# Kernel tuning notes

Hardware: AMD Instinct MI355X
Metric: run time of the kernel (lower is better)

The kernel has to match this reference:

```python
import jax, jax.numpy as jnp
import numpy as np
import math

NUM_HEADS = 16
SEGMENT_SIZE = 256
DILATION_RATE = 2


def _hilbert_curve(n):
    if n == 1:
        return [(0, 0)]
    m = n // 2
    sub = _hilbert_curve(m)
    pts = [(y, x) for (x, y) in sub]
    pts += [(x, y + m) for (x, y) in sub]
    pts += [(x + m, y + m) for (x, y) in sub]
    pts += [(m - 1 - y + m, m - 1 - x) for (x, y) in sub]
    return pts


def generate_hilbert_curve_mapping(seq_len):
    grid = 2 ** int(math.ceil(math.log2(math.sqrt(seq_len))))
    pts = _hilbert_curve(grid)
    lin2hil = np.zeros(seq_len, dtype=np.int32)
    for h_idx, (x, y) in enumerate(pts[:seq_len]):
        lin = y * grid + x
        if lin < seq_len:
            lin2hil[lin] = h_idx
    return lin2hil


def setup_inputs() -> dict:
    key = jax.random.key(0)
    k1, k2, k3 = jax.random.split(key, 3)
    B, S, H = 1, 4096, 2048
    scale = H ** -0.5
    x = jax.random.normal(k1, (B, S, H), dtype=jnp.float32)
    w_qkv = jax.random.normal(k2, (3 * H, H), dtype=jnp.float32) * scale
    w_out = jax.random.normal(k3, (H, H), dtype=jnp.float32) * scale
    hilbert_map = jnp.asarray(generate_hilbert_curve_mapping(S))
    return {"x": x, "w_qkv": w_qkv, "w_out": w_out, "hilbert_map": hilbert_map}


def _kv_positions(S, seg, dil):
    # Union of per-segment dilated positions: seg_start + j*dil (< segment end).
    seg_starts = np.arange(0, S, seg)
    within = np.arange(0, seg, dil)
    return jnp.asarray((seg_starts[:, None] + within[None, :]).reshape(-1))


def reference(x, w_qkv, w_out, hilbert_map):
    B, S, H = x.shape
    nh = NUM_HEADS
    hd = H // nh
    qkv = x @ w_qkv.T                              # [B,S,3H]
    qkv = qkv.reshape(B, S, 3, nh, hd).transpose(2, 0, 3, 1, 4)  # [3,B,nh,S,hd]
    q, k, v = qkv[0], qkv[1], qkv[2]

    kv_pos = _kv_positions(S, SEGMENT_SIZE, DILATION_RATE)  # [Nk]
    gathered = hilbert_map[kv_pos]                 # Hilbert-mapped KV indices
    kg = k[:, :, gathered, :]                      # [B,nh,Nk,hd]
    vg = v[:, :, gathered, :]

    scale = 1.0 / jnp.sqrt(jnp.float32(hd))
    scores = jnp.einsum("bhmd,bhnd->bhmn", q, kg) * scale
    p = jax.nn.softmax(scores, axis=-1)
    acc = jnp.einsum("bhmn,bhnd->bhmd", p, vg)     # [B,nh,S,hd]

    # Scatter: out[:, :, hilbert_map[m], :] = acc[:, :, m, :]
    out = jnp.zeros_like(acc).at[:, :, hilbert_map, :].set(acc)
    out = out.transpose(0, 2, 1, 3).reshape(B, S, H)
    return out @ w_out.T
```

## Files before the change

kernel.cpp:

```cpp
#include <hip/hip_runtime.h>
#include <math.h>

#define S_LEN 4096
#define HID   2048
#define NH    16
#define HD    128
#define NKV   2048
#define KT    64
#define QBLK  256
#define NT    (NKV / KT)
#define QSCALE 0.12754103668587426f

typedef __attribute__((ext_vector_type(8))) _Float16 half8;
typedef __attribute__((ext_vector_type(4))) _Float16 half4;
typedef __attribute__((ext_vector_type(2))) __fp16 fp16x2;
typedef __attribute__((ext_vector_type(4))) float f32x4;
typedef __attribute__((ext_vector_type(16))) float f32x16;

#define GLB_AS __attribute__((address_space(1)))
#define LDS_AS __attribute__((address_space(3)))

__device__ __forceinline__ void gload16(const void* g, void* l) {
  __builtin_amdgcn_global_load_lds((GLB_AS const void*)g, (LDS_AS void*)l, 16, 0, 0);
}

__device__ __forceinline__ unsigned pkrtz(float a, float b) {
  union { fp16x2 h; unsigned u; } cv;
  cv.h = __builtin_amdgcn_cvt_pkrtz(a, b);
  return cv.u;
}

__global__ void k_build_idx(const int* __restrict__ hmap, int* __restrict__ gidx) {
  int i = blockIdx.x * 256 + threadIdx.x;
  if (i < NKV) gidx[i] = hmap[2 * i];
}

__global__ void k_cvt_f16(const float* __restrict__ src, _Float16* __restrict__ dst, int n8) {
  int i = blockIdx.x * 256 + threadIdx.x;
  if (i < n8) {
    float4 a = ((const float4*)src)[2 * i];
    float4 b = ((const float4*)src)[2 * i + 1];
    half8 h;
    h[0] = (_Float16)a.x; h[1] = (_Float16)a.y; h[2] = (_Float16)a.z; h[3] = (_Float16)a.w;
    h[4] = (_Float16)b.x; h[5] = (_Float16)b.y; h[6] = (_Float16)b.z; h[7] = (_Float16)b.w;
    ((half8*)dst)[i] = h;
  }
}

template<int MODE>
__global__ __launch_bounds__(256)
void k_gemm2(const _Float16* __restrict__ A, const _Float16* __restrict__ B,
             void* __restrict__ Cv, int M, int N, int K,
             const int* __restrict__ arow,
             char* __restrict__ kimg, char* __restrict__ vtimg)
{
  __shared__ __align__(16) char Asl[16384];
  __shared__ __align__(16) char Bsl[16384];
  const int tid = threadIdx.x;
  const int w = tid >> 6, lane = tid & 63;
  const int l15 = lane & 15, l4 = lane >> 4;
  const int m0 = blockIdx.y * 128, n0 = blockIdx.x * 128;
  const int wr = w >> 1, wc = w & 1;

  const int srow  = lane >> 3;
  const int kso   = ((lane & 7) ^ srow) * 8;
  const _Float16* Ap[4];
  const _Float16* Bp[4];
#pragma unroll
  for (int q = 0; q < 4; ++q) {
    int arel = m0 + 32 * w + 8 * q + srow;
    int ra = arow ? arow[arel] : arel;
    Ap[q] = A + (size_t)ra * K + kso;
    Bp[q] = B + (size_t)(n0 + 32 * w + 8 * q + srow) * K + kso;
  }

  f32x4 acc[4][4];
#pragma unroll
  for (int i = 0; i < 4; ++i)
#pragma unroll
    for (int j = 0; j < 4; ++j) acc[i][j] = (f32x4){0.f, 0.f, 0.f, 0.f};

#define STAGE_T(k0)                                                  \
  do {                                                               \
    _Pragma("unroll")                                                \
    for (int q = 0; q < 4; ++q) {                                    \
      gload16(Ap[q] + (k0), Asl + (4 * w + q) * 1024 + lane * 16);   \
      gload16(Bp[q] + (k0), Bsl + (4 * w + q) * 1024 + lane * 16);   \
    }                                                                \
  } while (0)

  STAGE_T(0);
  __syncthreads();

  const int nt = K >> 6;
  for (int t = 0; t < nt; ++t) {
    half8 af[4][2], bf[4][2];
#pragma unroll
    for (int mi = 0; mi < 4; ++mi) {
      int row = wr * 64 + mi * 16 + l15;
#pragma unroll
      for (int ks = 0; ks < 2; ++ks)
        af[mi][ks] = *(const half8*)(Asl + row * 128 + (((ks * 4 + l4) ^ (row & 7)) * 16));
    }
#pragma unroll
    for (int ni = 0; ni < 4; ++ni) {
      int row = wc * 64 + ni * 16 + l15;
#pragma unroll
      for (int ks = 0; ks < 2; ++ks)
        bf[ni][ks] = *(const half8*)(Bsl + row * 128 + (((ks * 4 + l4) ^ (row & 7)) * 16));
    }
    __syncthreads();
    if (t + 1 < nt) STAGE_T((t + 1) * 64);
    __builtin_amdgcn_s_setprio(1);
#pragma unroll
    for (int mi = 0; mi < 4; ++mi)
#pragma unroll
      for (int ni = 0; ni < 4; ++ni)
#pragma unroll
        for (int ks = 0; ks < 2; ++ks)
          acc[mi][ni] = __builtin_amdgcn_mfma_f32_16x16x32_f16(af[mi][ks], bf[ni][ks], acc[mi][ni], 0, 0, 0);
    __builtin_amdgcn_s_setprio(0);
    __syncthreads();
  }
#undef STAGE_T

  const int rbase = m0 + wr * 64 + l4 * 4;
  const int cbase = n0 + wc * 64 + l15;
#pragma unroll
  for (int mi = 0; mi < 4; ++mi)
#pragma unroll
    for (int ni = 0; ni < 4; ++ni)
#pragma unroll
      for (int e = 0; e < 4; ++e) {
        int row = rbase + mi * 16 + e;
        int col = cbase + ni * 16;
        if (MODE == 1) {
          ((float*)Cv)[(size_t)row * N + col] = acc[mi][ni][e];
        } else if (MODE == 0) {
          ((_Float16*)Cv)[(size_t)row * N + col] = (_Float16)acc[mi][ni][e];
        } else {
          _Float16 val = (_Float16)acc[mi][ni][e];
          int t = row >> 6, j = row & 63;
          if (col < HID) {
            int h = col >> 7, d = col & 127;
            int off = (h * 32 + t) * 16384 + ((j * 256 + 2 * d) ^ ((j & 7) << 4));
            *(_Float16*)(kimg + off) = val;
          } else {
            int nn = col - HID;
            int h = nn >> 7, d = nn & 127;
            int off = (h * 32 + t) * 16384 + ((d * 128 + 2 * j) ^ ((d & 7) << 4));
            *(_Float16*)(vtimg + off) = val;
          }
        }
      }
}

__global__ __launch_bounds__(512, 2)
void k_attn7(const _Float16* __restrict__ qmat, const char* __restrict__ kimg,
             const char* __restrict__ vtimg, const int* __restrict__ hmap,
             _Float16* __restrict__ att)
{
  extern __shared__ __align__(16) char lds[];
  const int tid = threadIdx.x;
  const int w = tid >> 6, lane = tid & 63;
  const int l31 = lane & 31;
  const bool hi = (lane >> 5) != 0;
  const int hib = hi ? 1 : 0;
  const int work = (blockIdx.x & 7) * 32 + (blockIdx.x >> 3);
  const int h  = work >> 4;
  const int q0 = (work & 15) * QBLK;

  half8 qf[8];
  {
    const int qrow = q0 + w * 32 + l31;
    const _Float16* qb = qmat + (size_t)qrow * HID + h * HD + hib * 8;
    const _Float16 qs = (_Float16)QSCALE;
#pragma unroll
    for (int dk = 0; dk < 8; ++dk) {
      half8 v = *(const half8*)(qb + 16 * dk);
#pragma unroll
      for (int q = 0; q < 8; ++q) v[q] *= qs;
      qf[dk] = v;
    }
  }

  half8 ones;
#pragma unroll
  for (int q = 0; q < 8; ++q) ones[q] = (_Float16)1.0f;

  const int swz = (l31 & 7) << 4;
  int koff[4], voff[4];
#pragma unroll
  for (int i = 0; i < 4; ++i) {
    koff[i] = l31 * 256 + ((i * 32 + hib * 16) ^ swz);
    voff[i] = 16384 + l31 * 128 + ((i * 32 + hib * 16) ^ swz);
  }

  const char* kbase = kimg  + (size_t)h * NT * 16384;
  const char* vbase = vtimg + (size_t)h * NT * 16384;

  f32x16 acc[4];
  f32x16 accl;
#pragma unroll
  for (int dt = 0; dt < 4; ++dt)
#pragma unroll
    for (int r = 0; r < 16; ++r) acc[dt][r] = 0.f;
#pragma unroll
  for (int r = 0; r < 16; ++r) accl[r] = 0.f;

#define STAGE(buf, t)                                                          \
  do {                                                                         \
    const char* ks_ = kbase + (size_t)(t) * 16384;                             \
    const char* vs_ = vbase + (size_t)(t) * 16384;                             \
    char* d_ = lds + (buf) * 32768;                                            \
    gload16(ks_ + w * 1024 + lane * 16,          d_ + w * 1024);               \
    gload16(ks_ + (8 + w) * 1024 + lane * 16,    d_ + (8 + w) * 1024);         \
    gload16(vs_ + w * 1024 + lane * 16,          d_ + 16384 + w * 1024);       \
    gload16(vs_ + (8 + w) * 1024 + lane * 16,    d_ + 16384 + (8 + w) * 1024); \
  } while (0)

#define TILE(CUR, T)                                                           \
  do {                                                                         \
    if ((T) + 1 < NT) STAGE((CUR) ^ 1, (T) + 1);                               \
    f32x16 s[2];                                                               \
    __builtin_amdgcn_s_setprio(1);                                             \
    _Pragma("unroll")                                                          \
    for (int jt = 0; jt < 2; ++jt) {                                           \
      f32x16 ss;                                                               \
      _Pragma("unroll")                                                        \
      for (int r = 0; r < 16; ++r) ss[r] = 0.f;                                \
      _Pragma("unroll")                                                        \
      for (int dk = 0; dk < 8; ++dk) {                                         \
        half8 kf = *(const half8*)(lds + koff[dk & 3] +                        \
                    ((CUR) * 32768 + jt * 8192 + (dk >> 2) * 128));            \
        ss = __builtin_amdgcn_mfma_f32_32x32x16_f16(kf, qf[dk], ss, 0, 0, 0);  \
      }                                                                        \
      s[jt] = ss;                                                              \
    }                                                                          \
    __builtin_amdgcn_s_setprio(0);                                             \
    unsigned P_pk[2][4][2];                                                    \
    _Pragma("unroll")                                                          \
    for (int jt = 0; jt < 2; ++jt)                                             \
      _Pragma("unroll")                                                        \
      for (int rq = 0; rq < 4; ++rq)                                           \
        _Pragma("unroll")                                                      \
        for (int h2 = 0; h2 < 2; ++h2) {                                       \
          float p0 = exp2f(s[jt][4 * rq + 2 * h2]);                            \
          float p1 = exp2f(s[jt][4 * rq + 2 * h2 + 1]);                        \
          P_pk[jt][rq][h2] = pkrtz(p0, p1);                                    \
        }                                                                      \
    _Pragma("unroll")                                                          \
    for (int ks = 0; ks < 4; ++ks) {                                           \
      const int jt = ks >> 1, k1 = ks & 1;                                     \
      unsigned send0 = hi ? P_pk[jt][2 * k1][0]     : P_pk[jt][2 * k1 + 1][0]; \
      unsigned send1 = hi ? P_pk[jt][2 * k1][1]     : P_pk[jt][2 * k1 + 1][1]; \
      unsigned recv0 = (unsigned)__shfl_xor((int)send0, 32);                   \
      unsigned recv1 = (unsigned)__shfl_xor((int)send1, 32);                   \
      unsigned self0 = hi ? P_pk[jt][2 * k1 + 1][0] : P_pk[jt][2 * k1][0];     \
      unsigned self1 = hi ? P_pk[jt][2 * k1 + 1][1] : P_pk[jt][2 * k1][1];     \
      union { unsigned u[4]; half8 hv; } pf;                                   \
      pf.u[0] = hi ? recv0 : self0;                                            \
      pf.u[1] = hi ? recv1 : self1;                                            \
      pf.u[2] = hi ? self0 : recv0;                                            \
      pf.u[3] = hi ? self1 : recv1;                                            \
      __builtin_amdgcn_s_setprio(1);                                           \
      _Pragma("unroll")                                                        \
      for (int dt = 0; dt < 4; ++dt) {                                         \
        half8 vf = *(const half8*)(lds + voff[ks] +                            \
                    ((CUR) * 32768 + dt * 4096));                              \
        acc[dt] = __builtin_amdgcn_mfma_f32_32x32x16_f16(vf, pf.hv, acc[dt], 0, 0, 0); \
      }                                                                        \
      accl = __builtin_amdgcn_mfma_f32_32x32x16_f16(ones, pf.hv, accl, 0, 0, 0); \
      __builtin_amdgcn_s_setprio(0);                                           \
    }                                                                          \
    asm volatile("s_waitcnt vmcnt(0)");                                        \
    __syncthreads();                                                           \
  } while (0)

  STAGE(0, 0);
  asm volatile("s_waitcnt vmcnt(0)");
  __syncthreads();

  for (int t = 0; t < NT; t += 2) {
    TILE(0, t);
    TILE(1, t + 1);
  }
#undef TILE
#undef STAGE

  const float rl = 1.0f / accl[0];
  const int qrow = q0 + w * 32 + l31;
  const int srow = hmap[qrow];
  _Float16* ob = att + (size_t)srow * HID + h * HD;
#pragma unroll
  for (int dt = 0; dt < 4; ++dt)
#pragma unroll
    for (int rq = 0; rq < 4; ++rq) {
      const int d0 = dt * 32 + 8 * rq + 4 * hib;
      half4 o;
      o[0] = (_Float16)(acc[dt][4 * rq + 0] * rl);
      o[1] = (_Float16)(acc[dt][4 * rq + 1] * rl);
      o[2] = (_Float16)(acc[dt][4 * rq + 2] * rl);
      o[3] = (_Float16)(acc[dt][4 * rq + 3] * rl);
      *(half4*)(ob + d0) = o;
    }
}

extern "C" void kernel_launch(void* const* d_in, const int* in_sizes, int n_in,
                              void* d_out, int out_size, void* d_ws, size_t ws_size,
                              hipStream_t stream)
{
  const float* x     = (const float*)d_in[0];
  const float* w_qkv = (const float*)d_in[1];
  const float* w_out = (const float*)d_in[2];
  const int*   hmap  = (const int*)d_in[3];
  float* out = (float*)d_out;

  char* ws = (char*)d_ws;
  int* gidx = (int*)ws;                                          ws += 8192;
  _Float16* x16    = (_Float16*)ws;
  _Float16* att16  = (_Float16*)ws;                              ws += (size_t)S_LEN * HID * 2;
  _Float16* wqkv16 = (_Float16*)ws;                              ws += (size_t)3 * HID * HID * 2;
  _Float16* wout16 = (_Float16*)ws;                              ws += (size_t)HID * HID * 2;
  _Float16* q16    = (_Float16*)ws;                              ws += (size_t)S_LEN * HID * 2;
  char* kimg  = ws;                                              ws += (size_t)NH * NT * 16384;
  char* vtimg = ws;

  k_build_idx<<<8, 256, 0, stream>>>(hmap, gidx);

  k_cvt_f16<<<(S_LEN * HID / 8 + 255) / 256, 256, 0, stream>>>(x, x16, S_LEN * HID / 8);
  k_cvt_f16<<<(3 * HID * HID / 8 + 255) / 256, 256, 0, stream>>>(w_qkv, wqkv16, 3 * HID * HID / 8);
  k_cvt_f16<<<(HID * HID / 8 + 255) / 256, 256, 0, stream>>>(w_out, wout16, HID * HID / 8);

  dim3 gq(HID / 128, S_LEN / 128);
  k_gemm2<0><<<gq, 256, 0, stream>>>(x16, wqkv16, q16, S_LEN, HID, HID, nullptr, nullptr, nullptr);
  dim3 gkv(2 * HID / 128, NKV / 128);
  k_gemm2<2><<<gkv, 256, 0, stream>>>(x16, wqkv16 + (size_t)HID * HID, nullptr,
                                      NKV, 2 * HID, HID, gidx, kimg, vtimg);

  k_attn7<<<NH * (S_LEN / QBLK), 512, 65536, stream>>>(q16, kimg, vtimg, hmap, att16);

  dim3 go(HID / 128, S_LEN / 128);
  k_gemm2<1><<<go, 256, 0, stream>>>(att16, wout16, out, S_LEN, HID, HID, nullptr, nullptr, nullptr);
}
```

Baseline: 235.2 us.

## Split attention KV range across two blocks and merge partials in output GEMM

```diff
diff --git a/kernel.cpp b/kernel.cpp
--- a/kernel.cpp
+++ b/kernel.cpp
@@ -35,16 +35,29 @@
   if (i < NKV) gidx[i] = hmap[2 * i];
 }
 
-__global__ void k_cvt_f16(const float* __restrict__ src, _Float16* __restrict__ dst, int n8) {
+#define NX8  (S_LEN * HID / 8)
+#define NW8  (3 * HID * HID / 8)
+#define NO8  (HID * HID / 8)
+__global__ void k_cvt_all(const float* __restrict__ x, const float* __restrict__ wq,
+                          const float* __restrict__ wo, _Float16* __restrict__ x16,
+                          _Float16* __restrict__ wq16, _Float16* __restrict__ wo16) {
   int i = blockIdx.x * 256 + threadIdx.x;
-  if (i < n8) {
-    float4 a = ((const float4*)src)[2 * i];
-    float4 b = ((const float4*)src)[2 * i + 1];
-    half8 h;
-    h[0] = (_Float16)a.x; h[1] = (_Float16)a.y; h[2] = (_Float16)a.z; h[3] = (_Float16)a.w;
-    h[4] = (_Float16)b.x; h[5] = (_Float16)b.y; h[6] = (_Float16)b.z; h[7] = (_Float16)b.w;
-    ((half8*)dst)[i] = h;
-  }
+  const float* src; _Float16* dst; int j;
+  if (i < NX8)            { src = x;  dst = x16;  j = i; }
+  else if (i < NX8 + NW8) { src = wq; dst = wq16; j = i - NX8; }
+  else                    { src = wo; dst = wo16; j = i - NX8 - NW8; }
+  float4 a = ((const float4*)src)[2 * j];
+  float4 b = ((const float4*)src)[2 * j + 1];
+  half8 h;
+  h[0] = (_Float16)a.x; h[1] = (_Float16)a.y; h[2] = (_Float16)a.z; h[3] = (_Float16)a.w;
+  h[4] = (_Float16)b.x; h[5] = (_Float16)b.y; h[6] = (_Float16)b.z; h[7] = (_Float16)b.w;
+  ((half8*)dst)[j] = h;
+}
+
+__global__ void k_rl(const float* __restrict__ l0, const float* __restrict__ l1,
+                     _Float16* __restrict__ rlb) {
+  int i = blockIdx.x * 256 + threadIdx.x;
+  rlb[i] = (_Float16)(1.0f / (l0[i] + l1[i]));
 }
 
 template<int MODE>
@@ -134,9 +147,7 @@
       for (int e = 0; e < 4; ++e) {
         int row = rbase + mi * 16 + e;
         int col = cbase + ni * 16;
-        if (MODE == 1) {
-          ((float*)Cv)[(size_t)row * N + col] = acc[mi][ni][e];
-        } else if (MODE == 0) {
+        if (MODE == 0) {
           ((_Float16*)Cv)[(size_t)row * N + col] = (_Float16)acc[mi][ni][e];
         } else {
           _Float16 val = (_Float16)acc[mi][ni][e];
@@ -155,10 +166,106 @@
       }
 }
 
-__global__ __launch_bounds__(512, 2)
-void k_attn7(const _Float16* __restrict__ qmat, const char* __restrict__ kimg,
+__global__ __launch_bounds__(256)
+void k_gemm_out(const _Float16* __restrict__ A0, const _Float16* __restrict__ A1,
+                const _Float16* __restrict__ rlb, const _Float16* __restrict__ B,
+                float* __restrict__ C, int M, int N, int K)
+{
+  __shared__ __align__(16) char Asl[16384];
+  __shared__ __align__(16) char Bsl[16384];
+  const int tid = threadIdx.x;
+  const int w = tid >> 6, lane = tid & 63;
+  const int l15 = lane & 15, l4 = lane >> 4;
+  const int m0 = blockIdx.y * 128, n0 = blockIdx.x * 128;
+  const int wr = w >> 1, wc = w & 1;
+
+  const int srow  = lane >> 3;
+  const int kso   = ((lane & 7) ^ srow) * 8;
+  const _Float16* Ap0[4];
+  const _Float16* Ap1[4];
+  const _Float16* Bp[4];
+  const _Float16* Rp[4];
+#pragma unroll
+  for (int q = 0; q < 4; ++q) {
+    int row = m0 + 32 * w + 8 * q + srow;
+    Ap0[q] = A0 + (size_t)row * K + kso;
+    Ap1[q] = A1 + (size_t)row * K + kso;
+    Rp[q]  = rlb + row * NH;
+    Bp[q] = B + (size_t)(n0 + 32 * w + 8 * q + srow) * K + kso;
+  }
+
+  f32x4 acc[4][4];
+#pragma unroll
+  for (int i = 0; i < 4; ++i)
+#pragma unroll
+    for (int j = 0; j < 4; ++j) acc[i][j] = (f32x4){0.f, 0.f, 0.f, 0.f};
+
+#define STAGE_O(k0)                                                   \
+  do {                                                                \
+    _Pragma("unroll")                                                 \
+    for (int q = 0; q < 4; ++q) {                                     \
+      half8 v0 = *(const half8*)(Ap0[q] + (k0));                      \
+      half8 v1 = *(const half8*)(Ap1[q] + (k0));                      \
+      _Float16 rl = Rp[q][((k0) + kso) >> 7];                         \
+      half8 s = v0 + v1;                                              \
+      _Pragma("unroll")                                               \
+      for (int e = 0; e < 8; ++e) s[e] *= rl;                         \
+      *(half8*)(Asl + (4 * w + q) * 1024 + lane * 16) = s;            \
+      gload16(Bp[q] + (k0), Bsl + (4 * w + q) * 1024 + lane * 16);    \
+    }                                                                 \
+  } while (0)
+
+  STAGE_O(0);
+  __syncthreads();
+
+  const int nt = K >> 6;
+  for (int t = 0; t < nt; ++t) {
+    half8 af[4][2], bf[4][2];
+#pragma unroll
+    for (int mi = 0; mi < 4; ++mi) {
+      int row = wr * 64 + mi * 16 + l15;
+#pragma unroll
+      for (int ks = 0; ks < 2; ++ks)
+        af[mi][ks] = *(const half8*)(Asl + row * 128 + (((ks * 4 + l4) ^ (row & 7)) * 16));
+    }
+#pragma unroll
+    for (int ni = 0; ni < 4; ++ni) {
+      int row = wc * 64 + ni * 16 + l15;
+#pragma unroll
+      for (int ks = 0; ks < 2; ++ks)
+        bf[ni][ks] = *(const half8*)(Bsl + row * 128 + (((ks * 4 + l4) ^ (row & 7)) * 16));
+    }
+    __syncthreads();
+    if (t + 1 < nt) STAGE_O((t + 1) * 64);
+    __builtin_amdgcn_s_setprio(1);
+#pragma unroll
+    for (int mi = 0; mi < 4; ++mi)
+#pragma unroll
+      for (int ni = 0; ni < 4; ++ni)
+#pragma unroll
+        for (int ks = 0; ks < 2; ++ks)
+          acc[mi][ni] = __builtin_amdgcn_mfma_f32_16x16x32_f16(af[mi][ks], bf[ni][ks], acc[mi][ni], 0, 0, 0);
+    __builtin_amdgcn_s_setprio(0);
+    __syncthreads();
+  }
+#undef STAGE_O
+
+  const int rbase = m0 + wr * 64 + l4 * 4;
+  const int cbase = n0 + wc * 64 + l15;
+#pragma unroll
+  for (int mi = 0; mi < 4; ++mi)
+#pragma unroll
+    for (int ni = 0; ni < 4; ++ni)
+#pragma unroll
+      for (int e = 0; e < 4; ++e)
+        C[(size_t)(rbase + mi * 16 + e) * N + cbase + ni * 16] = acc[mi][ni][e];
+}
+
+__global__ __launch_bounds__(512, 4)
+void k_attn8(const _Float16* __restrict__ qmat, const char* __restrict__ kimg,
              const char* __restrict__ vtimg, const int* __restrict__ hmap,
-             _Float16* __restrict__ att)
+             _Float16* __restrict__ a0, _Float16* __restrict__ a1,
+             float* __restrict__ l0, float* __restrict__ l1)
 {
   extern __shared__ __align__(16) char lds[];
   const int tid = threadIdx.x;
@@ -166,9 +273,13 @@
   const int l31 = lane & 31;
   const bool hi = (lane >> 5) != 0;
   const int hib = hi ? 1 : 0;
-  const int work = (blockIdx.x & 7) * 32 + (blockIdx.x >> 3);
-  const int h  = work >> 4;
-  const int q0 = (work & 15) * QBLK;
+  const int work = (blockIdx.x & 7) * 64 + (blockIdx.x >> 3);
+  const int half = work & 1;
+  const int pi   = work >> 1;
+  const int h  = pi >> 4;
+  const int q0 = (pi & 15) * QBLK;
+  const int t0 = half * (NT / 2);
+  const int tend = t0 + NT / 2;
 
   half8 qf[8];
   {
@@ -221,7 +332,7 @@
 
 #define TILE(CUR, T)                                                           \
   do {                                                                         \
-    if ((T) + 1 < NT) STAGE((CUR) ^ 1, (T) + 1);                               \
+    if ((T) + 1 < tend) STAGE((CUR) ^ 1, (T) + 1);                             \
     f32x16 s[2];                                                               \
     __builtin_amdgcn_s_setprio(1);                                             \
     _Pragma("unroll")                                                          \
@@ -277,33 +388,33 @@
     __syncthreads();                                                           \
   } while (0)
 
-  STAGE(0, 0);
+  STAGE(0, t0);
   asm volatile("s_waitcnt vmcnt(0)");
   __syncthreads();
 
-  for (int t = 0; t < NT; t += 2) {
+  for (int t = t0; t < tend; t += 2) {
     TILE(0, t);
     TILE(1, t + 1);
   }
 #undef TILE
 #undef STAGE
 
-  const float rl = 1.0f / accl[0];
   const int qrow = q0 + w * 32 + l31;
   const int srow = hmap[qrow];
-  _Float16* ob = att + (size_t)srow * HID + h * HD;
+  _Float16* ob = (half ? a1 : a0) + (size_t)srow * HID + h * HD;
 #pragma unroll
   for (int dt = 0; dt < 4; ++dt)
 #pragma unroll
     for (int rq = 0; rq < 4; ++rq) {
       const int d0 = dt * 32 + 8 * rq + 4 * hib;
       half4 o;
-      o[0] = (_Float16)(acc[dt][4 * rq + 0] * rl);
-      o[1] = (_Float16)(acc[dt][4 * rq + 1] * rl);
-      o[2] = (_Float16)(acc[dt][4 * rq + 2] * rl);
-      o[3] = (_Float16)(acc[dt][4 * rq + 3] * rl);
+      o[0] = (_Float16)acc[dt][4 * rq + 0];
+      o[1] = (_Float16)acc[dt][4 * rq + 1];
+      o[2] = (_Float16)acc[dt][4 * rq + 2];
+      o[3] = (_Float16)acc[dt][4 * rq + 3];
       *(half4*)(ob + d0) = o;
     }
+  if (!hi) (half ? l1 : l0)[srow * NH + h] = accl[0];
 }
 
 extern "C" void kernel_launch(void* const* d_in, const int* in_sizes, int n_in,
@@ -319,18 +430,20 @@
   char* ws = (char*)d_ws;
   int* gidx = (int*)ws;                                          ws += 8192;
   _Float16* x16    = (_Float16*)ws;
-  _Float16* att16  = (_Float16*)ws;                              ws += (size_t)S_LEN * HID * 2;
+  _Float16* a0     = (_Float16*)ws;                              ws += (size_t)S_LEN * HID * 2;
+  _Float16* a1     = (_Float16*)ws;                              ws += (size_t)S_LEN * HID * 2;
   _Float16* wqkv16 = (_Float16*)ws;                              ws += (size_t)3 * HID * HID * 2;
   _Float16* wout16 = (_Float16*)ws;                              ws += (size_t)HID * HID * 2;
   _Float16* q16    = (_Float16*)ws;                              ws += (size_t)S_LEN * HID * 2;
   char* kimg  = ws;                                              ws += (size_t)NH * NT * 16384;
-  char* vtimg = ws;
+  char* vtimg = ws;                                              ws += (size_t)NH * NT * 16384;
+  float* l0   = (float*)ws;                                      ws += S_LEN * NH * 4;
+  float* l1   = (float*)ws;                                      ws += S_LEN * NH * 4;
+  _Float16* rlb = (_Float16*)ws;
 
   k_build_idx<<<8, 256, 0, stream>>>(hmap, gidx);
-
-  k_cvt_f16<<<(S_LEN * HID / 8 + 255) / 256, 256, 0, stream>>>(x, x16, S_LEN * HID / 8);
-  k_cvt_f16<<<(3 * HID * HID / 8 + 255) / 256, 256, 0, stream>>>(w_qkv, wqkv16, 3 * HID * HID / 8);
-  k_cvt_f16<<<(HID * HID / 8 + 255) / 256, 256, 0, stream>>>(w_out, wout16, HID * HID / 8);
+  k_cvt_all<<<(NX8 + NW8 + NO8 + 255) / 256, 256, 0, stream>>>(x, w_qkv, w_out,
+                                                               x16, wqkv16, wout16);
 
   dim3 gq(HID / 128, S_LEN / 128);
   k_gemm2<0><<<gq, 256, 0, stream>>>(x16, wqkv16, q16, S_LEN, HID, HID, nullptr, nullptr, nullptr);
@@ -338,8 +451,10 @@
   k_gemm2<2><<<gkv, 256, 0, stream>>>(x16, wqkv16 + (size_t)HID * HID, nullptr,
                                       NKV, 2 * HID, HID, gidx, kimg, vtimg);
 
-  k_attn7<<<NH * (S_LEN / QBLK), 512, 65536, stream>>>(q16, kimg, vtimg, hmap, att16);
+  k_attn8<<<2 * NH * (S_LEN / QBLK), 512, 65536, stream>>>(q16, kimg, vtimg, hmap,
+                                                           a0, a1, l0, l1);
+  k_rl<<<S_LEN * NH / 256, 256, 0, stream>>>(l0, l1, rlb);
 
   dim3 go(HID / 128, S_LEN / 128);
-  k_gemm2<1><<<go, 256, 0, stream>>>(att16, wout16, out, S_LEN, HID, HID, nullptr, nullptr, nullptr);
-}
+  k_gemm_out<<<go, 256, 0, stream>>>(a0, a1, rlb, wout16, out, S_LEN, HID, HID);
+}
```

New measurement: 514.6 us. +118.8%, slower.
